# Kernel tuning notes

Hardware: AMD Instinct MI355X
Metric: run time of the kernel (lower is better)

The kernel has to match this reference:

```python
import jax, jax.numpy as jnp
import numpy as np

B, C, N = 4, 256, 4096
OUT = 256
TEMP = OUT ** 0.5  # temperature = sqrt(out_channel)


def setup_inputs() -> dict:
    key = jax.random.key(0)
    kx, kxx, kq, kk, kv = jax.random.split(key, 5)
    x = jax.random.normal(kx, (B, C, N), dtype=jnp.float32)
    xx = jax.random.normal(kxx, (B, C, N), dtype=jnp.float32)
    # Conv1d(in, out, kernel=1, bias=False) weights, squeezed to (out, in)
    s = 1.0 / np.sqrt(C)
    Wq = jax.random.uniform(kq, (OUT, C), jnp.float32, -s, s)
    Wk = jax.random.uniform(kk, (OUT, C), jnp.float32, -s, s)
    Wv = jax.random.uniform(kv, (OUT, C), jnp.float32, -s, s)
    return {"x": x, "xx": xx, "Wq": Wq, "Wk": Wk, "Wv": Wv}


def reference(x, xx, Wq, Wk, Wv):
    # 1x1 conv == per-point linear: (out,in) x (b,in,n) -> (b,out,n)
    q = jnp.einsum('oc,bcn->bon', Wq, x)
    k = jnp.einsum('oc,bcn->bon', Wk, xx)
    v = jnp.einsum('oc,bcn->bon', Wv, xx)
    # attn = (q^T / temp) @ k : (B, N, N)
    attn = jax.nn.softmax(jnp.einsum('bon,bom->bnm', q, k) / TEMP, axis=-1)
    # dropout is identity in eval mode
    # y = attn @ v^T -> (B, N, OUT); returned transposed to (B, OUT, N)
    y = jnp.einsum('bnm,bom->bon', attn, v)
    return y
```

## Files before the change

### kernel.cpp

```cpp
#include <hip/hip_runtime.h>
#include <hip/hip_bf16.h>


typedef __attribute__((ext_vector_type(8))) short bf16x8;
typedef __attribute__((ext_vector_type(4))) float f32x4;
typedef __attribute__((ext_vector_type(4))) short short4t;

constexpr int B_ = 4;
constexpr int C_ = 256;
constexpr int N_ = 4096;
constexpr int O_ = 256;
constexpr float INV_TEMP = 1.0f / 16.0f;
constexpr int NIT = 64;

__device__ __forceinline__ short f2bf(float f) {
  union { float f; unsigned u; } v; v.f = f;
  unsigned r = v.u + 0x7fffu + ((v.u >> 16) & 1u);
  return (short)(r >> 16);
}

__device__ __forceinline__ void dma16(const short* g, short* l) {
  __builtin_amdgcn_global_load_lds(
      (const __attribute__((address_space(1))) unsigned int*)g,
      (__attribute__((address_space(3))) unsigned int*)l, 16, 0, 0);
}

__global__ void wcvt(const float* __restrict__ Wq, const float* __restrict__ Wk,
                     const float* __restrict__ Wv, short* __restrict__ wb) {
  int i = blockIdx.x * 256 + threadIdx.x;
  int mat = i >> 16, off = i & 65535;
  const float* W = (mat == 0) ? Wq : (mat == 1 ? Wk : Wv);
  wb[i] = f2bf(W[off]);
}

__global__ __launch_bounds__(256, 2) void qkv_proj(
    const float* __restrict__ x, const float* __restrict__ xx,
    const short* __restrict__ wb,
    short* __restrict__ qg, short* __restrict__ kt, short* __restrict__ vt) {
  const int n0  = blockIdx.x * 64;
  const int b   = blockIdx.y;
  const int mat = blockIdx.z;
  const float* src = (mat == 0) ? x : xx;
  const short* W   = wb + mat * 65536;
  const int tid = threadIdx.x;
  const int w = tid >> 6, lane = tid & 63;
  const int g = lane >> 4, c16 = lane & 15;

  __shared__ __align__(16) short xs[64][264];

  {
    const int n = tid & 63, cq = tid >> 6;
    const float* sp = src + (size_t)b * C_ * N_ + n0 + n;
#pragma unroll
    for (int rep = 0; rep < 16; ++rep) {
      int c = rep * 16 + cq * 4;
      short4t s4;
#pragma unroll
      for (int j = 0; j < 4; ++j) s4[j] = f2bf(sp[(size_t)(c + j) * N_]);
      *(short4t*)&xs[n][c] = s4;
    }
  }
  __syncthreads();

  f32x4 acc[4][4];
#pragma unroll
  for (int i = 0; i < 4; ++i)
#pragma unroll
    for (int j = 0; j < 4; ++j) acc[i][j] = (f32x4){0.f, 0.f, 0.f, 0.f};

#pragma unroll
  for (int ko = 0; ko < 8; ++ko) {
    bf16x8 wfr[4], xfr[4];
#pragma unroll
    for (int ot = 0; ot < 4; ++ot)
      wfr[ot] = *(const bf16x8*)&W[(w * 64 + ot * 16 + c16) * C_ + ko * 32 + g * 8];
#pragma unroll
    for (int nt = 0; nt < 4; ++nt)
      xfr[nt] = *(const bf16x8*)&xs[nt * 16 + c16][ko * 32 + g * 8];
    if (mat < 2) {
#pragma unroll
      for (int ot = 0; ot < 4; ++ot)
#pragma unroll
        for (int nt = 0; nt < 4; ++nt)
          acc[ot][nt] = __builtin_amdgcn_mfma_f32_16x16x32_bf16(
              wfr[ot], xfr[nt], acc[ot][nt], 0, 0, 0);
    } else {
#pragma unroll
      for (int mt = 0; mt < 4; ++mt)
#pragma unroll
        for (int ot = 0; ot < 4; ++ot)
          acc[mt][ot] = __builtin_amdgcn_mfma_f32_16x16x32_bf16(
              xfr[mt], wfr[ot], acc[mt][ot], 0, 0, 0);
    }
  }

  __syncthreads();
  short* ob = &xs[0][0];

  if (mat == 0) {
#pragma unroll
    for (int ot = 0; ot < 4; ++ot)
#pragma unroll
      for (int nt = 0; nt < 4; ++nt) {
        int f = (nt * 16 + c16) * 256 + w * 64 + ot * 16 + g * 4;
        short4t s;
        s[0] = f2bf(acc[ot][nt][0] * INV_TEMP);
        s[1] = f2bf(acc[ot][nt][1] * INV_TEMP);
        s[2] = f2bf(acc[ot][nt][2] * INV_TEMP);
        s[3] = f2bf(acc[ot][nt][3] * INV_TEMP);
        *(short4t*)&ob[f] = s;
      }
  } else if (mat == 1) {
#pragma unroll
    for (int ot = 0; ot < 4; ++ot)
#pragma unroll
      for (int nt = 0; nt < 4; ++nt) {
        int koo = w * 2 + (ot >> 1);
        int pos = (((ot & 1) * 2 + (g >> 1)) ^ ((c16 >> 1) & 3));
        int f = nt * 4096 + koo * 512 + c16 * 32 + pos * 8 + (g & 1) * 4;
        short4t s;
        s[0] = f2bf(acc[ot][nt][0]);
        s[1] = f2bf(acc[ot][nt][1]);
        s[2] = f2bf(acc[ot][nt][2]);
        s[3] = f2bf(acc[ot][nt][3]);
        *(short4t*)&ob[f] = s;
      }
  } else {
#pragma unroll
    for (int mt = 0; mt < 4; ++mt)
#pragma unroll
      for (int ot = 0; ot < 4; ++ot) {
        int o = w * 64 + ot * 16 + c16;
        int pos = (mt * 2 + (g >> 1)) ^ (o & 7);
        int f = o * 64 + pos * 8 + (g & 1) * 4;
        short4t s;
        s[0] = f2bf(acc[mt][ot][0]);
        s[1] = f2bf(acc[mt][ot][1]);
        s[2] = f2bf(acc[mt][ot][2]);
        s[3] = f2bf(acc[mt][ot][3]);
        *(short4t*)&ob[f] = s;
      }
  }
  __syncthreads();

  short* dst = (mat == 0) ? qg + ((size_t)b * N_ + n0) * O_
             : (mat == 1) ? kt + (size_t)(b * 256 + (n0 >> 4)) * 4096
                          : vt + (size_t)(b * 64 + (n0 >> 6)) * 16384;
  const uint4* s4 = (const uint4*)ob;
  uint4* d4 = (uint4*)dst;
#pragma unroll
  for (int j = 0; j < 8; ++j) d4[j * 256 + tid] = s4[j * 256 + tid];
}

__global__ __launch_bounds__(512, 2) void flash_attn(
    const short* __restrict__ qg, const short* __restrict__ kt,
    const short* __restrict__ vt, float* __restrict__ out) {
  const int xg = blockIdx.x;
  const int b  = xg >> 1;
  const int n0 = (((xg & 1) << 5) + blockIdx.y) * 64;
  const int tid = threadIdx.x;
  const int w = tid >> 6, lane = tid & 63;
  const int g = lane >> 4, c16 = lane & 15;
  const bool prod = (w < 4);
  const int pw = w & 3;

  __shared__ short kb[2][16384];
  __shared__ short vb[2][16384];
  __shared__ short ps[2][64][72];
  __shared__ float lsum[4][64];

  const short* ktb = kt + (size_t)b * N_ * O_;
  const short* vtb = vt + (size_t)b * N_ * O_;

  bf16x8 qf[4][8];
  float lrun[4] = {0.f, 0.f, 0.f, 0.f};
  f32x4 oacc[4][4];
#pragma unroll
  for (int i = 0; i < 4; ++i)
#pragma unroll
    for (int j = 0; j < 4; ++j) oacc[i][j] = (f32x4){0.f, 0.f, 0.f, 0.f};

  if (prod) {
#pragma unroll
    for (int nt = 0; nt < 4; ++nt) {
      const short* qrow =
          qg + (size_t)(b * N_ + n0 + nt * 16 + c16) * O_ + g * 8;
#pragma unroll
      for (int ko = 0; ko < 8; ++ko)
        qf[nt][ko] = *(const bf16x8*)(qrow + ko * 32);
    }
    const short* src = ktb + (size_t)pw * 4096;
#pragma unroll
    for (int j = 0; j < 8; ++j)
      dma16(src + j * 512 + lane * 8, &kb[0][pw * 4096 + j * 512]);
  }
  __syncthreads();

  const int sw = (g ^ ((c16 >> 1) & 3)) * 8;

  for (int i = 0; i <= NIT; ++i) {
    if (prod) {
      if (i < NIT) {
        if (i + 1 < NIT) {
          const short* src = ktb + (size_t)(4 * (i + 1) + pw) * 4096;
          short* dst = &kb[(i + 1) & 1][pw * 4096];
#pragma unroll
          for (int j = 0; j < 8; ++j)
            dma16(src + j * 512 + lane * 8, dst + j * 512);
        }
        const short* ksl = &kb[i & 1][pw * 4096];
        f32x4 sacc[4];
#pragma unroll
        for (int nt = 0; nt < 4; ++nt) sacc[nt] = (f32x4){0.f, 0.f, 0.f, 0.f};
#pragma unroll
        for (int ko = 0; ko < 8; ++ko) {
          bf16x8 kf = *(const bf16x8*)&ksl[(ko * 16 + c16) * 32 + sw];
#pragma unroll
          for (int nt = 0; nt < 4; ++nt)
            sacc[nt] = __builtin_amdgcn_mfma_f32_16x16x32_bf16(
                kf, qf[nt][ko], sacc[nt], 0, 0, 0);
        }
#pragma unroll
        for (int nt = 0; nt < 4; ++nt) {
          short4t pb;
          float rs = 0.f;
#pragma unroll
          for (int r = 0; r < 4; ++r) {
            float p = __expf(sacc[nt][r]);
            rs += p;
            pb[r] = f2bf(p);
          }
          lrun[nt] += rs;
          *(short4t*)&ps[i & 1][nt * 16 + c16][pw * 16 + g * 4] = pb;
        }
      }
    } else {
      if (i < NIT) {
        const short* src = vtb + (size_t)i * 16384 + pw * 4096;
        short* dst = &vb[i & 1][pw * 4096];
#pragma unroll
        for (int j = 0; j < 8; ++j)
          dma16(src + j * 512 + lane * 8, dst + j * 512);
      }
      if (i > 0) {
        const int pb_ = (i - 1) & 1;
#pragma unroll
        for (int kk = 0; kk < 2; ++kk) {
          bf16x8 pf[4];
#pragma unroll
          for (int nt = 0; nt < 4; ++nt)
            pf[nt] = *(const bf16x8*)&ps[pb_][nt * 16 + c16][kk * 32 + g * 8];
#pragma unroll
          for (int ot = 0; ot < 4; ++ot) {
            int pos = (kk * 4 + g) ^ (c16 & 7);
            bf16x8 vf = *(const bf16x8*)
                &vb[pb_][(pw * 64 + ot * 16 + c16) * 64 + pos * 8];
#pragma unroll
            for (int nt = 0; nt < 4; ++nt)
              oacc[ot][nt] = __builtin_amdgcn_mfma_f32_16x16x32_bf16(
                  vf, pf[nt], oacc[ot][nt], 0, 0, 0);
          }
        }
      }
    }
    __syncthreads();
  }

  if (prod) {
#pragma unroll
    for (int nt = 0; nt < 4; ++nt) {
      float v = lrun[nt];
      v += __shfl_xor(v, 16);
      v += __shfl_xor(v, 32);
      if (lane < 16) lsum[pw][nt * 16 + lane] = v;
    }
  }
  __syncthreads();
  if (!prod) {
#pragma unroll
    for (int nt = 0; nt < 4; ++nt) {
      const int nl = nt * 16 + c16;
      float l = lsum[0][nl] + lsum[1][nl] + lsum[2][nl] + lsum[3][nl];
      float li = 1.0f / l;
#pragma unroll
      for (int ot = 0; ot < 4; ++ot) {
        float* op = out + ((size_t)b * O_ + pw * 64 + ot * 16 + g * 4) * N_ +
                    n0 + nl;
#pragma unroll
        for (int r = 0; r < 4; ++r)
          op[(size_t)r * N_] = oacc[ot][nt][r] * li;
      }
    }
  }
}

extern "C" void kernel_launch(void* const* d_in, const int* in_sizes, int n_in,
                              void* d_out, int out_size, void* d_ws,
                              size_t ws_size, hipStream_t stream) {
  const float* x  = (const float*)d_in[0];
  const float* xx = (const float*)d_in[1];
  const float* Wq = (const float*)d_in[2];
  const float* Wk = (const float*)d_in[3];
  const float* Wv = (const float*)d_in[4];
  float* out = (float*)d_out;

  short* qg = (short*)d_ws;
  short* kt = qg + (size_t)B_ * N_ * O_;
  short* vt = kt + (size_t)B_ * N_ * O_;
  short* wb = vt + (size_t)B_ * N_ * O_;

  wcvt<<<768, 256, 0, stream>>>(Wq, Wk, Wv, wb);
  qkv_proj<<<dim3(N_ / 64, B_, 3), 256, 0, stream>>>(x, xx, wb, qg, kt, vt);
  flash_attn<<<dim3(8, 32), 512, 0, stream>>>(qg, kt, vt, out);
}
```

Measured before the change: 205.0 us.

## Load K and V tiles directly from global into registers, bypassing LDS

Drops the LDS double buffers for K and V. Each producer and consumer wave now loads its K or V fragments straight from global memory into registers, issued one iteration ahead as a register prefetch. The per-iteration sync is replaced with an LDS-only waitcnt plus a raw barrier, and the MFMA loops are wrapped in s_setprio raises. This is meant to cut LDS traffic, shared memory footprint and the cost of waiting on vmcnt at the barrier. In exchange it adds register pressure and exposes global load latency if the prefetch distance is too short.

After: 263.6 us. +28.6%, slower.

```diff
diff --git a/kernel.cpp b/kernel.cpp
--- a/kernel.cpp
+++ b/kernel.cpp
@@ -17,12 +17,6 @@
   union { float f; unsigned u; } v; v.f = f;
   unsigned r = v.u + 0x7fffu + ((v.u >> 16) & 1u);
   return (short)(r >> 16);
-}
-
-__device__ __forceinline__ void dma16(const short* g, short* l) {
-  __builtin_amdgcn_global_load_lds(
-      (const __attribute__((address_space(1))) unsigned int*)g,
-      (__attribute__((address_space(3))) unsigned int*)l, 16, 0, 0);
 }
 
 __global__ void wcvt(const float* __restrict__ Wq, const float* __restrict__ Wk,
@@ -164,8 +158,6 @@
   const bool prod = (w < 4);
   const int pw = w & 3;
 
-  __shared__ short kb[2][16384];
-  __shared__ short vb[2][16384];
   __shared__ short ps[2][64][72];
   __shared__ float lsum[4][64];
 
@@ -173,12 +165,16 @@
   const short* vtb = vt + (size_t)b * N_ * O_;
 
   bf16x8 qf[4][8];
+  bf16x8 kf[8];
+  bf16x8 vf[8];
   float lrun[4] = {0.f, 0.f, 0.f, 0.f};
   f32x4 oacc[4][4];
 #pragma unroll
   for (int i = 0; i < 4; ++i)
 #pragma unroll
     for (int j = 0; j < 4; ++j) oacc[i][j] = (f32x4){0.f, 0.f, 0.f, 0.f};
+
+  const int koff = c16 * 32 + ((g ^ ((c16 >> 1) & 3)) * 8);
 
   if (prod) {
 #pragma unroll
@@ -189,36 +185,33 @@
       for (int ko = 0; ko < 8; ++ko)
         qf[nt][ko] = *(const bf16x8*)(qrow + ko * 32);
     }
-    const short* src = ktb + (size_t)pw * 4096;
+    const short* kg = ktb + (size_t)pw * 4096;
 #pragma unroll
     for (int j = 0; j < 8; ++j)
-      dma16(src + j * 512 + lane * 8, &kb[0][pw * 4096 + j * 512]);
-  }
-  __syncthreads();
-
-  const int sw = (g ^ ((c16 >> 1) & 3)) * 8;
+      kf[j] = *(const bf16x8*)(kg + j * 512 + koff);
+  }
+  __syncthreads();
 
   for (int i = 0; i <= NIT; ++i) {
     if (prod) {
       if (i < NIT) {
-        if (i + 1 < NIT) {
-          const short* src = ktb + (size_t)(4 * (i + 1) + pw) * 4096;
-          short* dst = &kb[(i + 1) & 1][pw * 4096];
-#pragma unroll
-          for (int j = 0; j < 8; ++j)
-            dma16(src + j * 512 + lane * 8, dst + j * 512);
-        }
-        const short* ksl = &kb[i & 1][pw * 4096];
         f32x4 sacc[4];
 #pragma unroll
         for (int nt = 0; nt < 4; ++nt) sacc[nt] = (f32x4){0.f, 0.f, 0.f, 0.f};
+        __builtin_amdgcn_s_setprio(1);
 #pragma unroll
         for (int ko = 0; ko < 8; ++ko) {
-          bf16x8 kf = *(const bf16x8*)&ksl[(ko * 16 + c16) * 32 + sw];
 #pragma unroll
           for (int nt = 0; nt < 4; ++nt)
             sacc[nt] = __builtin_amdgcn_mfma_f32_16x16x32_bf16(
-                kf, qf[nt][ko], sacc[nt], 0, 0, 0);
+                kf[ko], qf[nt][ko], sacc[nt], 0, 0, 0);
+        }
+        __builtin_amdgcn_s_setprio(0);
+        if (i + 1 < NIT) {
+          const short* kg = ktb + (size_t)(4 * (i + 1) + pw) * 4096;
+#pragma unroll
+          for (int j = 0; j < 8; ++j)
+            kf[j] = *(const bf16x8*)(kg + j * 512 + koff);
         }
 #pragma unroll
         for (int nt = 0; nt < 4; ++nt) {
@@ -235,15 +228,9 @@
         }
       }
     } else {
-      if (i < NIT) {
-        const short* src = vtb + (size_t)i * 16384 + pw * 4096;
-        short* dst = &vb[i & 1][pw * 4096];
-#pragma unroll
-        for (int j = 0; j < 8; ++j)
-          dma16(src + j * 512 + lane * 8, dst + j * 512);
-      }
       if (i > 0) {
         const int pb_ = (i - 1) & 1;
+        __builtin_amdgcn_s_setprio(1);
 #pragma unroll
         for (int kk = 0; kk < 2; ++kk) {
           bf16x8 pf[4];
@@ -252,18 +239,27 @@
             pf[nt] = *(const bf16x8*)&ps[pb_][nt * 16 + c16][kk * 32 + g * 8];
 #pragma unroll
           for (int ot = 0; ot < 4; ++ot) {
-            int pos = (kk * 4 + g) ^ (c16 & 7);
-            bf16x8 vf = *(const bf16x8*)
-                &vb[pb_][(pw * 64 + ot * 16 + c16) * 64 + pos * 8];
 #pragma unroll
             for (int nt = 0; nt < 4; ++nt)
               oacc[ot][nt] = __builtin_amdgcn_mfma_f32_16x16x32_bf16(
-                  vf, pf[nt], oacc[ot][nt], 0, 0, 0);
+                  vf[kk * 4 + ot], pf[nt], oacc[ot][nt], 0, 0, 0);
           }
         }
-      }
-    }
-    __syncthreads();
+        __builtin_amdgcn_s_setprio(0);
+      }
+      if (i < NIT) {
+        const short* vg = vtb + (size_t)i * 16384;
+#pragma unroll
+        for (int kk = 0; kk < 2; ++kk)
+#pragma unroll
+          for (int ot = 0; ot < 4; ++ot)
+            vf[kk * 4 + ot] = *(const bf16x8*)(
+                vg + (pw * 64 + ot * 16 + c16) * 64 +
+                ((kk * 4 + g) ^ (c16 & 7)) * 8);
+      }
+    }
+    asm volatile("s_waitcnt lgkmcnt(0)" ::: "memory");
+    __builtin_amdgcn_s_barrier();
   }
 
   if (prod) {
```
